# Optimization experiments

Hardware: AMD Instinct MI355X
Metric: run time of the kernel (lower is better)

The kernel has to match this reference:

```python
import jax, jax.numpy as jnp
import numpy as np

N = 8192
F_IN = 512
F_HID = 256
ALPHA = 0.2  # LeakyReLU negative slope
NEG_INF = -9e15


def gat_layer(h, adj, W, a):
    """Standard dense GraphAttentionLayer (pyGAT style).
    h: [N, F_in], adj: [N, N] (0/1), W: [F_in, F_out], a: [2*F_out, 1].
    """
    Wh = h @ W  # [N, F_out]
    f_out = W.shape[1]
    # e_ij = leakyrelu(a1 . Wh_i + a2 . Wh_j) via broadcasting
    e1 = Wh @ a[:f_out]      # [N, 1]
    e2 = Wh @ a[f_out:]      # [N, 1]
    e = jax.nn.leaky_relu(e1 + e2.T, negative_slope=ALPHA)  # [N, N]
    e = jnp.where(adj > 0, e, NEG_INF)
    att = jax.nn.softmax(e, axis=-1)  # masked row softmax
    return jax.nn.elu(att @ Wh)       # [N, F_out]


def setup_inputs() -> dict:
    key = jax.random.key(0)
    k_x, k_adj, k_w1, k_a1, k_w2, k_a2 = jax.random.split(key, 6)
    x = jax.random.normal(k_x, (N, F_IN), dtype=jnp.float32)
    # sparse random adjacency (~avg degree 16) + self loops
    adj = (jax.random.uniform(k_adj, (N, N)) < (16.0 / N)).astype(jnp.float32)
    adj = jnp.clip(adj + jnp.eye(N, dtype=jnp.float32), 0.0, 1.0)
    # Xavier-ish init for layer params
    W1 = jax.random.normal(k_w1, (F_IN, F_HID), dtype=jnp.float32) * (1.0 / np.sqrt(F_IN))
    a1 = jax.random.normal(k_a1, (2 * F_HID, 1), dtype=jnp.float32) * (1.0 / np.sqrt(2 * F_HID))
    W2 = jax.random.normal(k_w2, (F_HID, F_IN), dtype=jnp.float32) * (1.0 / np.sqrt(F_HID))
    a2 = jax.random.normal(k_a2, (2 * F_IN, 1), dtype=jnp.float32) * (1.0 / np.sqrt(2 * F_IN))
    return {"x": x, "adj": adj, "W1": W1, "a1": a1, "W2": W2, "a2": a2}


def reference(x, adj, W1, a1, W2, a2):
    enc = gat_layer(x, adj, W1, a1)    # encode: [N, F_HID]
    dec = gat_layer(enc, adj, W2, a2)  # decode: [N, F_IN]
    return (dec, enc)
```

## Files before the change

### kernel.cpp

```cpp
#include <hip/hip_runtime.h>
#include <hip/hip_bf16.h>

#define N_NODES 8192
#define F_IN    512
#define F_HID   256
#define ALPHA   0.2f
#define MAXDEG  64

using f32x4 = __attribute__((ext_vector_type(4))) float;
using f16x8 = __attribute__((ext_vector_type(8))) _Float16;
using f16x4 = __attribute__((ext_vector_type(4))) _Float16;

__global__ void conv_WT(const float* __restrict__ W1, const float* __restrict__ W2,
                        _Float16* __restrict__ W1T, _Float16* __restrict__ W2T) {
    int t = blockIdx.x;
    const float* W; _Float16* WT; int K, N, kt, nt;
    if (t < 128) { W = W1; WT = W1T; K = 512; N = 256; kt = t & 15; nt = t >> 4; }
    else { t -= 128; W = W2; WT = W2T; K = 256; N = 512; kt = t & 7; nt = t >> 3; }
    __shared__ float Ws[32][33];
    const int tx = threadIdx.x & 31, ty = threadIdx.x >> 5;
    #pragma unroll
    for (int i = 0; i < 4; ++i)
        Ws[ty + 8 * i][tx] = W[(size_t)(kt * 32 + ty + 8 * i) * N + nt * 32 + tx];
    __syncthreads();
    #pragma unroll
    for (int i = 0; i < 4; ++i)
        WT[(size_t)(nt * 32 + ty + 8 * i) * K + kt * 32 + tx] = (_Float16)Ws[tx][ty + 8 * i];
}

__device__ inline void csr_row(const float* __restrict__ adj, int* __restrict__ cols,
                               int* __restrict__ cnt, int row, int lane) {
    const float4* arow = (const float4*)(adj + (size_t)row * N_NODES);
    int* crow = cols + (size_t)row * MAXDEG;
    int count = 0;
    const unsigned long long mlt = (1ULL << lane) - 1ULL;
    for (int base = 0; base < N_NODES; base += 256) {
        float4 v = arow[(base >> 2) + lane];
        unsigned long long b0 = __ballot(v.x > 0.0f);
        unsigned long long b1 = __ballot(v.y > 0.0f);
        unsigned long long b2 = __ballot(v.z > 0.0f);
        unsigned long long b3 = __ballot(v.w > 0.0f);
        int o = count + __popcll(b0 & mlt) + __popcll(b1 & mlt)
                      + __popcll(b2 & mlt) + __popcll(b3 & mlt);
        int c0 = base + (lane << 2);
        if (v.x > 0.0f) { if (o < MAXDEG) crow[o] = c0;     o++; }
        if (v.y > 0.0f) { if (o < MAXDEG) crow[o] = c0 + 1; o++; }
        if (v.z > 0.0f) { if (o < MAXDEG) crow[o] = c0 + 2; o++; }
        if (v.w > 0.0f) { if (o < MAXDEG) crow[o] = c0 + 3; o++; }
        count += __popcll(b0) + __popcll(b1) + __popcll(b2) + __popcll(b3);
    }
    if (lane == 0) cnt[row] = count > MAXDEG ? MAXDEG : count;
}

__device__ inline void gemm1_tile(const float* __restrict__ x,
                                  const _Float16* __restrict__ W1T,
                                  _Float16* __restrict__ Wh1,
                                  int brow, int bcol) {
    const int LDT = 72;
    __shared__ _Float16 As[64 * LDT];
    __shared__ _Float16 Bs[64 * LDT];
    const int tid = threadIdx.x;
    const int wid = tid >> 6, lane = tid & 63;
    const int wr = (wid >> 1) * 32, wc = (wid & 1) * 32;
    const int sr = tid >> 3, skg = (tid & 7) * 8;

    f32x4 acc[2][2];
    #pragma unroll
    for (int m = 0; m < 2; ++m)
        #pragma unroll
        for (int n = 0; n < 2; ++n) acc[m][n] = f32x4{0.f, 0.f, 0.f, 0.f};

    for (int k0 = 0; k0 < F_IN; k0 += 64) {
        #pragma unroll
        for (int i = 0; i < 2; ++i) {
            int r = sr + i * 32;
            const float* src = x + (size_t)(brow + r) * F_IN + k0 + skg;
            f32x4 a0 = *(const f32x4*)src;
            f32x4 a1 = *(const f32x4*)(src + 4);
            f16x8 av;
            #pragma unroll
            for (int j = 0; j < 4; ++j) { av[j] = (_Float16)a0[j]; av[4 + j] = (_Float16)a1[j]; }
            *(f16x8*)&As[r * LDT + skg] = av;
            *(f16x8*)&Bs[r * LDT + skg] = *(const f16x8*)&W1T[(size_t)(bcol + r) * F_IN + k0 + skg];
        }
        __syncthreads();
        #pragma unroll
        for (int ks = 0; ks < 2; ++ks) {
            const int kb = ks * 32 + (lane >> 4) * 8;
            f16x8 af[2], bfr[2];
            #pragma unroll
            for (int m = 0; m < 2; ++m)
                af[m] = *(const f16x8*)&As[(wr + m * 16 + (lane & 15)) * LDT + kb];
            #pragma unroll
            for (int n = 0; n < 2; ++n)
                bfr[n] = *(const f16x8*)&Bs[(wc + n * 16 + (lane & 15)) * LDT + kb];
            #pragma unroll
            for (int m = 0; m < 2; ++m)
                #pragma unroll
                for (int n = 0; n < 2; ++n)
                    acc[m][n] = __builtin_amdgcn_mfma_f32_16x16x32_f16(
                        af[m], bfr[n], acc[m][n], 0, 0, 0);
        }
        __syncthreads();
    }
    #pragma unroll
    for (int m = 0; m < 2; ++m)
        #pragma unroll
        for (int n = 0; n < 2; ++n) {
            int row = brow + wr + m * 16 + ((lane >> 4) << 2);
            int col = bcol + wc + n * 16 + (lane & 15);
            #pragma unroll
            for (int j = 0; j < 4; ++j)
                Wh1[(size_t)(row + j) * F_HID + col] = (_Float16)acc[m][n][j];
        }
}

__global__ __launch_bounds__(256)
void csr_and_gemm1(const float* __restrict__ adj, int* __restrict__ cols,
                   int* __restrict__ cnt, const float* __restrict__ x,
                   const _Float16* __restrict__ W1T, _Float16* __restrict__ Wh1) {
    const int bid = blockIdx.x;
    const int g = bid / 5, r = bid % 5;
    if (r == 0) {
        gemm1_tile(x, W1T, Wh1, (g >> 2) * 64, (g & 3) * 64);
    } else {
        const int cb = g * 4 + (r - 1);
        const int row = cb * 4 + (threadIdx.x >> 6);
        csr_row(adj, cols, cnt, row, threadIdx.x & 63);
    }
}

__global__ __launch_bounds__(256)
void gemm2_f16(const _Float16* __restrict__ A, const _Float16* __restrict__ BT,
               _Float16* __restrict__ C) {
    const int LDT = 72;
    __shared__ _Float16 As[64 * LDT];
    __shared__ _Float16 Bs[64 * LDT];
    const int tid = threadIdx.x;
    const int wid = tid >> 6, lane = tid & 63;
    const int brow = (blockIdx.x >> 3) * 64;
    const int bcol = (blockIdx.x & 7) * 64;
    const int wr = (wid >> 1) * 32, wc = (wid & 1) * 32;
    const int sr = tid >> 3, skg = (tid & 7) * 8;

    f32x4 acc[2][2];
    #pragma unroll
    for (int m = 0; m < 2; ++m)
        #pragma unroll
        for (int n = 0; n < 2; ++n) acc[m][n] = f32x4{0.f, 0.f, 0.f, 0.f};

    for (int k0 = 0; k0 < F_HID; k0 += 64) {
        #pragma unroll
        for (int i = 0; i < 2; ++i) {
            int r = sr + i * 32;
            *(f16x8*)&As[r * LDT + skg] = *(const f16x8*)&A[(size_t)(brow + r) * F_HID + k0 + skg];
            *(f16x8*)&Bs[r * LDT + skg] = *(const f16x8*)&BT[(size_t)(bcol + r) * F_HID + k0 + skg];
        }
        __syncthreads();
        #pragma unroll
        for (int ks = 0; ks < 2; ++ks) {
            const int kb = ks * 32 + (lane >> 4) * 8;
            f16x8 af[2], bfr[2];
            #pragma unroll
            for (int m = 0; m < 2; ++m)
                af[m] = *(const f16x8*)&As[(wr + m * 16 + (lane & 15)) * LDT + kb];
            #pragma unroll
            for (int n = 0; n < 2; ++n)
                bfr[n] = *(const f16x8*)&Bs[(wc + n * 16 + (lane & 15)) * LDT + kb];
            #pragma unroll
            for (int m = 0; m < 2; ++m)
                #pragma unroll
                for (int n = 0; n < 2; ++n)
                    acc[m][n] = __builtin_amdgcn_mfma_f32_16x16x32_f16(
                        af[m], bfr[n], acc[m][n], 0, 0, 0);
        }
        __syncthreads();
    }
    #pragma unroll
    for (int m = 0; m < 2; ++m)
        #pragma unroll
        for (int n = 0; n < 2; ++n) {
            int row = brow + wr + m * 16 + ((lane >> 4) << 2);
            int col = bcol + wc + n * 16 + (lane & 15);
            #pragma unroll
            for (int j = 0; j < 4; ++j)
                C[(size_t)(row + j) * F_IN + col] = (_Float16)acc[m][n][j];
        }
}

template<int F>
__global__ void compute_st16(const _Float16* __restrict__ Wh, const float* __restrict__ a,
                             float* __restrict__ s, float* __restrict__ t) {
    const int EL = F / 64;
    const int lane = threadIdx.x & 63;
    const int row = blockIdx.x * 4 + (threadIdx.x >> 6);
    const _Float16* wr = Wh + (size_t)row * F + lane * EL;
    float ss = 0.f, tt = 0.f;
    #pragma unroll
    for (int c = 0; c < EL / 4; ++c) {
        f16x4 w = *(const f16x4*)(wr + c * 4);
        f32x4 a0 = *(const f32x4*)(a + lane * EL + c * 4);
        f32x4 a1 = *(const f32x4*)(a + F + lane * EL + c * 4);
        #pragma unroll
        for (int j = 0; j < 4; ++j) {
            float v = (float)w[j];
            ss += v * a0[j];
            tt += v * a1[j];
        }
    }
    #pragma unroll
    for (int off = 32; off > 0; off >>= 1) {
        ss += __shfl_xor(ss, off);
        tt += __shfl_xor(tt, off);
    }
    if (lane == 0) { s[row] = ss; t[row] = tt; }
}

template<int F>
__global__ void aggregate16(const _Float16* __restrict__ Wh,
                            const int* __restrict__ cols, const int* __restrict__ cnt,
                            const float* __restrict__ s, const float* __restrict__ t,
                            float* __restrict__ out, _Float16* __restrict__ out16) {
    const int EL = F / 64;
    const int wid = threadIdx.x >> 6, lane = threadIdx.x & 63;
    const int row = blockIdx.x * 4 + wid;
    const int deg = cnt[row];
    __shared__ float pS[4][64];
    __shared__ int jS[4][64];
    int j = 0;
    float ev = -1e30f;
    if (lane < deg) {
        j = cols[(size_t)row * MAXDEG + lane];
        float z = s[row] + t[j];
        ev = z > 0.0f ? z : ALPHA * z;
    }
    float m = ev;
    #pragma unroll
    for (int off = 32; off > 0; off >>= 1) m = fmaxf(m, __shfl_xor(m, off));
    float ex = (lane < deg) ? __expf(ev - m) : 0.0f;
    float sum = ex;
    #pragma unroll
    for (int off = 32; off > 0; off >>= 1) sum += __shfl_xor(sum, off);
    pS[wid][lane] = ex / sum;
    jS[wid][lane] = j;
    __syncthreads();

    float acc[EL] = {};
    #pragma unroll 2
    for (int d = 0; d < deg; ++d) {
        float p = pS[wid][d];
        const _Float16* wr = Wh + (size_t)jS[wid][d] * F + lane * EL;
        if constexpr (EL == 8) {
            f16x8 w = *(const f16x8*)wr;
            #pragma unroll
            for (int jj = 0; jj < 8; ++jj) acc[jj] += p * (float)w[jj];
        } else {
            f16x4 w = *(const f16x4*)wr;
            #pragma unroll
            for (int jj = 0; jj < 4; ++jj) acc[jj] += p * (float)w[jj];
        }
    }
    #pragma unroll
    for (int c = 0; c < EL / 4; ++c) {
        f32x4 o; f16x4 h;
        #pragma unroll
        for (int jj = 0; jj < 4; ++jj) {
            float v = acc[c * 4 + jj];
            float e = v > 0.0f ? v : (__expf(v) - 1.0f);
            o[jj] = e; h[jj] = (_Float16)e;
        }
        *(f32x4*)(out + (size_t)row * F + lane * EL + c * 4) = o;
        if (out16)
            *(f16x4*)(out16 + (size_t)row * F + lane * EL + c * 4) = h;
    }
}

extern "C" void kernel_launch(void* const* d_in, const int* in_sizes, int n_in,
                              void* d_out, int out_size, void* d_ws, size_t ws_size,
                              hipStream_t stream) {
    (void)in_sizes; (void)n_in; (void)out_size; (void)ws_size;
    const float* x   = (const float*)d_in[0];
    const float* adj = (const float*)d_in[1];
    const float* W1  = (const float*)d_in[2];
    const float* a1  = (const float*)d_in[3];
    const float* W2  = (const float*)d_in[4];
    const float* a2  = (const float*)d_in[5];

    float* dec = (float*)d_out;
    float* enc = dec + (size_t)N_NODES * F_IN;

    int*      cols  = (int*)d_ws;
    int*      cnt   = cols + (size_t)N_NODES * MAXDEG;
    float*    sbuf  = (float*)(cnt + N_NODES);
    float*    tbuf  = sbuf + N_NODES;
    _Float16* Wh1   = (_Float16*)(tbuf + N_NODES);
    _Float16* Wh2   = Wh1 + (size_t)N_NODES * F_HID;
    _Float16* enc16 = Wh2 + (size_t)N_NODES * F_IN;
    _Float16* W1T   = enc16 + (size_t)N_NODES * F_HID;
    _Float16* W2T   = W1T + (size_t)F_HID * F_IN;

    conv_WT<<<256, 256, 0, stream>>>(W1, W2, W1T, W2T);

    csr_and_gemm1<<<2560, 256, 0, stream>>>(adj, cols, cnt, x, W1T, Wh1);

    compute_st16<F_HID><<<N_NODES / 4, 256, 0, stream>>>(Wh1, a1, sbuf, tbuf);
    aggregate16<F_HID><<<N_NODES / 4, 256, 0, stream>>>(Wh1, cols, cnt, sbuf, tbuf, enc, enc16);

    gemm2_f16<<<1024, 256, 0, stream>>>(enc16, W2T, Wh2);
    compute_st16<F_IN><<<N_NODES / 4, 256, 0, stream>>>(Wh2, a2, sbuf, tbuf);
    aggregate16<F_IN><<<N_NODES / 4, 256, 0, stream>>>(Wh2, cols, cnt, sbuf, tbuf, dec, (_Float16*)nullptr);
}
```

Baseline: 115.4 us.

## Fuse attention score projections into GEMM epilogues, enlarge GEMM2 tile, unroll aggregation

The s/t attention projections are now computed inside the GEMM epilogues from the fp32 accumulators. Each epilogue reduces across lanes with shuffles and accumulates per-row partial sums with atomics into buffers that conv_WT zero-fills. This removes both compute_st16 kernels and the extra re-reads of Wh. GEMM2 now uses 128x64 tiles for more reuse per block and half the grid size, and the aggregation loop is unrolled by four to issue more independent gathers at once. The atomics make the s/t sums order-nondeterministic, and the scores now come from fp32 values rather than fp16-rounded ones.

```diff
diff --git a/kernel.cpp b/kernel.cpp
--- a/kernel.cpp
+++ b/kernel.cpp
@@ -12,7 +12,11 @@
 using f16x4 = __attribute__((ext_vector_type(4))) _Float16;
 
 __global__ void conv_WT(const float* __restrict__ W1, const float* __restrict__ W2,
-                        _Float16* __restrict__ W1T, _Float16* __restrict__ W2T) {
+                        _Float16* __restrict__ W1T, _Float16* __restrict__ W2T,
+                        float* __restrict__ stz) {
+    int gid = blockIdx.x * blockDim.x + threadIdx.x;
+    if (gid < 4 * N_NODES) stz[gid] = 0.0f;
+
     int t = blockIdx.x;
     const float* W; _Float16* WT; int K, N, kt, nt;
     if (t < 128) { W = W1; WT = W1T; K = 512; N = 256; kt = t & 15; nt = t >> 4; }
@@ -55,6 +59,8 @@
 __device__ inline void gemm1_tile(const float* __restrict__ x,
                                   const _Float16* __restrict__ W1T,
                                   _Float16* __restrict__ Wh1,
+                                  const float* __restrict__ a1,
+                                  float* __restrict__ s1, float* __restrict__ t1,
                                   int brow, int bcol) {
     const int LDT = 72;
     __shared__ _Float16 As[64 * LDT];
@@ -76,10 +82,10 @@
             int r = sr + i * 32;
             const float* src = x + (size_t)(brow + r) * F_IN + k0 + skg;
             f32x4 a0 = *(const f32x4*)src;
-            f32x4 a1 = *(const f32x4*)(src + 4);
+            f32x4 a1v = *(const f32x4*)(src + 4);
             f16x8 av;
             #pragma unroll
-            for (int j = 0; j < 4; ++j) { av[j] = (_Float16)a0[j]; av[4 + j] = (_Float16)a1[j]; }
+            for (int j = 0; j < 4; ++j) { av[j] = (_Float16)a0[j]; av[4 + j] = (_Float16)a1v[j]; }
             *(f16x8*)&As[r * LDT + skg] = av;
             *(f16x8*)&Bs[r * LDT + skg] = *(const f16x8*)&W1T[(size_t)(bcol + r) * F_IN + k0 + skg];
         }
@@ -103,8 +109,26 @@
         }
         __syncthreads();
     }
-    #pragma unroll
-    for (int m = 0; m < 2; ++m)
+    const int c0 = bcol + wc + (lane & 15);
+    float as0 = a1[c0],      as1 = a1[c0 + 16];
+    float at0 = a1[F_HID + c0], at1 = a1[F_HID + c0 + 16];
+    #pragma unroll
+    for (int m = 0; m < 2; ++m) {
+        #pragma unroll
+        for (int j = 0; j < 4; ++j) {
+            float vs = acc[m][0][j] * as0 + acc[m][1][j] * as1;
+            float vt = acc[m][0][j] * at0 + acc[m][1][j] * at1;
+            #pragma unroll
+            for (int off = 1; off < 16; off <<= 1) {
+                vs += __shfl_xor(vs, off);
+                vt += __shfl_xor(vt, off);
+            }
+            if ((lane & 15) == 0) {
+                int row = brow + wr + m * 16 + ((lane >> 4) << 2) + j;
+                atomicAdd(s1 + row, vs);
+                atomicAdd(t1 + row, vt);
+            }
+        }
         #pragma unroll
         for (int n = 0; n < 2; ++n) {
             int row = brow + wr + m * 16 + ((lane >> 4) << 2);
@@ -113,16 +137,19 @@
             for (int j = 0; j < 4; ++j)
                 Wh1[(size_t)(row + j) * F_HID + col] = (_Float16)acc[m][n][j];
         }
+    }
 }
 
 __global__ __launch_bounds__(256)
 void csr_and_gemm1(const float* __restrict__ adj, int* __restrict__ cols,
                    int* __restrict__ cnt, const float* __restrict__ x,
-                   const _Float16* __restrict__ W1T, _Float16* __restrict__ Wh1) {
+                   const _Float16* __restrict__ W1T, _Float16* __restrict__ Wh1,
+                   const float* __restrict__ a1,
+                   float* __restrict__ s1, float* __restrict__ t1) {
     const int bid = blockIdx.x;
     const int g = bid / 5, r = bid % 5;
     if (r == 0) {
-        gemm1_tile(x, W1T, Wh1, (g >> 2) * 64, (g & 3) * 64);
+        gemm1_tile(x, W1T, Wh1, a1, s1, t1, (g >> 2) * 64, (g & 3) * 64);
     } else {
         const int cb = g * 4 + (r - 1);
         const int row = cb * 4 + (threadIdx.x >> 6);
@@ -132,43 +159,46 @@
 
 __global__ __launch_bounds__(256)
 void gemm2_f16(const _Float16* __restrict__ A, const _Float16* __restrict__ BT,
-               _Float16* __restrict__ C) {
+               _Float16* __restrict__ C, const float* __restrict__ a2,
+               float* __restrict__ s2, float* __restrict__ t2) {
     const int LDT = 72;
-    __shared__ _Float16 As[64 * LDT];
+    __shared__ _Float16 As[128 * LDT];
     __shared__ _Float16 Bs[64 * LDT];
     const int tid = threadIdx.x;
     const int wid = tid >> 6, lane = tid & 63;
-    const int brow = (blockIdx.x >> 3) * 64;
+    const int brow = (blockIdx.x >> 3) * 128;
     const int bcol = (blockIdx.x & 7) * 64;
-    const int wr = (wid >> 1) * 32, wc = (wid & 1) * 32;
+    const int wr = (wid >> 1) * 64, wc = (wid & 1) * 32;
     const int sr = tid >> 3, skg = (tid & 7) * 8;
 
-    f32x4 acc[2][2];
-    #pragma unroll
-    for (int m = 0; m < 2; ++m)
+    f32x4 acc[4][2];
+    #pragma unroll
+    for (int m = 0; m < 4; ++m)
         #pragma unroll
         for (int n = 0; n < 2; ++n) acc[m][n] = f32x4{0.f, 0.f, 0.f, 0.f};
 
     for (int k0 = 0; k0 < F_HID; k0 += 64) {
         #pragma unroll
-        for (int i = 0; i < 2; ++i) {
+        for (int i = 0; i < 4; ++i) {
             int r = sr + i * 32;
             *(f16x8*)&As[r * LDT + skg] = *(const f16x8*)&A[(size_t)(brow + r) * F_HID + k0 + skg];
-            *(f16x8*)&Bs[r * LDT + skg] = *(const f16x8*)&BT[(size_t)(bcol + r) * F_HID + k0 + skg];
+            if (i < 2)
+                *(f16x8*)&Bs[(r & 63) * LDT + skg] =
+                    *(const f16x8*)&BT[(size_t)(bcol + (r & 63)) * F_HID + k0 + skg];
         }
         __syncthreads();
         #pragma unroll
         for (int ks = 0; ks < 2; ++ks) {
             const int kb = ks * 32 + (lane >> 4) * 8;
-            f16x8 af[2], bfr[2];
-            #pragma unroll
-            for (int m = 0; m < 2; ++m)
+            f16x8 af[4], bfr[2];
+            #pragma unroll
+            for (int m = 0; m < 4; ++m)
                 af[m] = *(const f16x8*)&As[(wr + m * 16 + (lane & 15)) * LDT + kb];
             #pragma unroll
             for (int n = 0; n < 2; ++n)
                 bfr[n] = *(const f16x8*)&Bs[(wc + n * 16 + (lane & 15)) * LDT + kb];
             #pragma unroll
-            for (int m = 0; m < 2; ++m)
+            for (int m = 0; m < 4; ++m)
                 #pragma unroll
                 for (int n = 0; n < 2; ++n)
                     acc[m][n] = __builtin_amdgcn_mfma_f32_16x16x32_f16(
@@ -176,8 +206,26 @@
         }
         __syncthreads();
     }
-    #pragma unroll
-    for (int m = 0; m < 2; ++m)
+    const int c0 = bcol + wc + (lane & 15);
+    float as0 = a2[c0],        as1 = a2[c0 + 16];
+    float at0 = a2[F_IN + c0], at1 = a2[F_IN + c0 + 16];
+    #pragma unroll
+    for (int m = 0; m < 4; ++m) {
+        #pragma unroll
+        for (int j = 0; j < 4; ++j) {
+            float vs = acc[m][0][j] * as0 + acc[m][1][j] * as1;
+            float vt = acc[m][0][j] * at0 + acc[m][1][j] * at1;
+            #pragma unroll
+            for (int off = 1; off < 16; off <<= 1) {
+                vs += __shfl_xor(vs, off);
+                vt += __shfl_xor(vt, off);
+            }
+            if ((lane & 15) == 0) {
+                int row = brow + wr + m * 16 + ((lane >> 4) << 2) + j;
+                atomicAdd(s2 + row, vs);
+                atomicAdd(t2 + row, vt);
+            }
+        }
         #pragma unroll
         for (int n = 0; n < 2; ++n) {
             int row = brow + wr + m * 16 + ((lane >> 4) << 2);
@@ -186,34 +234,7 @@
             for (int j = 0; j < 4; ++j)
                 C[(size_t)(row + j) * F_IN + col] = (_Float16)acc[m][n][j];
         }
-}
-
-template<int F>
-__global__ void compute_st16(const _Float16* __restrict__ Wh, const float* __restrict__ a,
-                             float* __restrict__ s, float* __restrict__ t) {
-    const int EL = F / 64;
-    const int lane = threadIdx.x & 63;
-    const int row = blockIdx.x * 4 + (threadIdx.x >> 6);
-    const _Float16* wr = Wh + (size_t)row * F + lane * EL;
-    float ss = 0.f, tt = 0.f;
-    #pragma unroll
-    for (int c = 0; c < EL / 4; ++c) {
-        f16x4 w = *(const f16x4*)(wr + c * 4);
-        f32x4 a0 = *(const f32x4*)(a + lane * EL + c * 4);
-        f32x4 a1 = *(const f32x4*)(a + F + lane * EL + c * 4);
-        #pragma unroll
-        for (int j = 0; j < 4; ++j) {
-            float v = (float)w[j];
-            ss += v * a0[j];
-            tt += v * a1[j];
-        }
-    }
-    #pragma unroll
-    for (int off = 32; off > 0; off >>= 1) {
-        ss += __shfl_xor(ss, off);
-        tt += __shfl_xor(tt, off);
-    }
-    if (lane == 0) { s[row] = ss; t[row] = tt; }
+    }
 }
 
 template<int F>
@@ -246,10 +267,34 @@
     __syncthreads();
 
     float acc[EL] = {};
-    #pragma unroll 2
-    for (int d = 0; d < deg; ++d) {
+    const size_t lo = (size_t)lane * EL;
+    int d = 0;
+    for (; d + 4 <= deg; d += 4) {
+        float p0 = pS[wid][d],     p1 = pS[wid][d + 1];
+        float p2 = pS[wid][d + 2], p3 = pS[wid][d + 3];
+        const _Float16* w0 = Wh + (size_t)jS[wid][d] * F + lo;
+        const _Float16* w1 = Wh + (size_t)jS[wid][d + 1] * F + lo;
+        const _Float16* w2 = Wh + (size_t)jS[wid][d + 2] * F + lo;
+        const _Float16* w3 = Wh + (size_t)jS[wid][d + 3] * F + lo;
+        if constexpr (EL == 8) {
+            f16x8 v0 = *(const f16x8*)w0, v1 = *(const f16x8*)w1;
+            f16x8 v2 = *(const f16x8*)w2, v3 = *(const f16x8*)w3;
+            #pragma unroll
+            for (int jj = 0; jj < 8; ++jj)
+                acc[jj] += p0 * (float)v0[jj] + p1 * (float)v1[jj]
+                         + p2 * (float)v2[jj] + p3 * (float)v3[jj];
+        } else {
+            f16x4 v0 = *(const f16x4*)w0, v1 = *(const f16x4*)w1;
+            f16x4 v2 = *(const f16x4*)w2, v3 = *(const f16x4*)w3;
+            #pragma unroll
+            for (int jj = 0; jj < 4; ++jj)
+                acc[jj] += p0 * (float)v0[jj] + p1 * (float)v1[jj]
+                         + p2 * (float)v2[jj] + p3 * (float)v3[jj];
+        }
+    }
+    for (; d < deg; ++d) {
         float p = pS[wid][d];
-        const _Float16* wr = Wh + (size_t)jS[wid][d] * F + lane * EL;
+        const _Float16* wr = Wh + (size_t)jS[wid][d] * F + lo;
         if constexpr (EL == 8) {
             f16x8 w = *(const f16x8*)wr;
             #pragma unroll
@@ -269,9 +314,9 @@
             float e = v > 0.0f ? v : (__expf(v) - 1.0f);
             o[jj] = e; h[jj] = (_Float16)e;
         }
-        *(f32x4*)(out + (size_t)row * F + lane * EL + c * 4) = o;
+        *(f32x4*)(out + (size_t)row * F + lo + c * 4) = o;
         if (out16)
-            *(f16x4*)(out16 + (size_t)row * F + lane * EL + c * 4) = h;
+            *(f16x4*)(out16 + (size_t)row * F + lo + c * 4) = h;
     }
 }
 
@@ -291,22 +336,23 @@
 
     int*      cols  = (int*)d_ws;
     int*      cnt   = cols + (size_t)N_NODES * MAXDEG;
-    float*    sbuf  = (float*)(cnt + N_NODES);
-    float*    tbuf  = sbuf + N_NODES;
-    _Float16* Wh1   = (_Float16*)(tbuf + N_NODES);
+    float*    s1    = (float*)(cnt + N_NODES);
+    float*    t1    = s1 + N_NODES;
+    float*    s2    = t1 + N_NODES;
+    float*    t2    = s2 + N_NODES;
+    _Float16* Wh1   = (_Float16*)(t2 + N_NODES);
     _Float16* Wh2   = Wh1 + (size_t)N_NODES * F_HID;
     _Float16* enc16 = Wh2 + (size_t)N_NODES * F_IN;
     _Float16* W1T   = enc16 + (size_t)N_NODES * F_HID;
     _Float16* W2T   = W1T + (size_t)F_HID * F_IN;
 
-    conv_WT<<<256, 256, 0, stream>>>(W1, W2, W1T, W2T);
-
-    csr_and_gemm1<<<2560, 256, 0, stream>>>(adj, cols, cnt, x, W1T, Wh1);
-
-    compute_st16<F_HID><<<N_NODES / 4, 256, 0, stream>>>(Wh1, a1, sbuf, tbuf);
-    aggregate16<F_HID><<<N_NODES / 4, 256, 0, stream>>>(Wh1, cols, cnt, sbuf, tbuf, enc, enc16);
-
-    gemm2_f16<<<1024, 256, 0, stream>>>(enc16, W2T, Wh2);
-    compute_st16<F_IN><<<N_NODES / 4, 256, 0, stream>>>(Wh2, a2, sbuf, tbuf);
-    aggregate16<F_IN><<<N_NODES / 4, 256, 0, stream>>>(Wh2, cols, cnt, sbuf, tbuf, dec, (_Float16*)nullptr);
-}
+    conv_WT<<<256, 256, 0, stream>>>(W1, W2, W1T, W2T, s1);
+
+    csr_and_gemm1<<<2560, 256, 0, stream>>>(adj, cols, cnt, x, W1T, Wh1, a1, s1, t1);
+
+    aggregate16<F_HID><<<N_NODES / 4, 256, 0, stream>>>(Wh1, cols, cnt, s1, t1, enc, enc16);
+
+    gemm2_f16<<<512, 256, 0, stream>>>(enc16, W2T, Wh2, a2, s2, t2);
+
+    aggregate16<F_IN><<<N_NODES / 4, 256, 0, stream>>>(Wh2, cols, cnt, s2, t2, dec, (_Float16*)nullptr);
+}
```

Result: faster. 113.1 us (-2.0%).
